# Kernel tuning notes

Hardware: AMD Instinct MI355X
Metric: run time of the kernel (lower is better)

The kernel has to match this reference:

```python
import jax, jax.numpy as jnp
import numpy as np

B = 16384
IN = 1024
H = 1024
LN_EPS = 1e-5


def setup_inputs() -> dict:
    key = jax.random.key(0)
    ks = jax.random.split(key, 8)
    # Five gate Linears fused into one weight [IN+H, 5H] (order: f, i, o, c, m)
    scale = 1.0 / np.sqrt(IN + H)
    W = jax.random.uniform(ks[0], (IN + H, 5 * H), jnp.float32, -scale, scale)
    b = jax.random.uniform(ks[1], (5 * H,), jnp.float32, -scale, scale)
    return {
        "x": jax.random.normal(ks[2], (B, IN), jnp.float32),
        "h_prev": jax.random.normal(ks[3], (B, H), jnp.float32),
        "c_prev": jax.random.normal(ks[4], (B, H), jnp.float32),
        "W": W,
        "b": b,
        "ln_gamma": jnp.ones((H,), jnp.float32),
        "ln_beta": jnp.zeros((H,), jnp.float32),
        "retention": jnp.full((H,), 0.9, jnp.float32),
    }


def _layernorm(z, gamma, beta):
    mu = jnp.mean(z, axis=-1, keepdims=True)
    var = jnp.var(z, axis=-1, keepdims=True)
    return (z - mu) * jax.lax.rsqrt(var + LN_EPS) * gamma + beta


def reference(x, h_prev, c_prev, W, b, ln_gamma, ln_beta, retention):
    combined = jnp.concatenate([x, h_prev], axis=-1)        # [B, IN+H]
    gates = combined @ W + b                                # [B, 5H] fused GEMM
    f_pre, i_pre, o_pre, c_pre_act, m_pre = jnp.split(gates, 5, axis=-1)
    f_gate = jax.nn.sigmoid(f_pre)
    i_gate = jax.nn.sigmoid(i_pre)
    o_gate = jax.nn.sigmoid(o_pre)
    c_cand = jnp.tanh(c_pre_act)
    m_gate = jax.nn.sigmoid(m_pre)
    c_new = f_gate * c_prev + i_gate * c_cand
    c_new = c_new * retention + (1.0 - retention) * c_prev
    c_new = m_gate * c_new + (1.0 - m_gate) * c_prev
    # exp(ln)/(1+exp(ln)) == sigmoid(layernorm(o_gate))
    o_exp = jax.nn.sigmoid(_layernorm(o_gate, ln_gamma, ln_beta))
    h_new = o_exp * jnp.tanh(c_new)
    return h_new, c_new
```

## Files before the change

kernel.cpp:

```cpp
#include <hip/hip_runtime.h>
#include <math.h>


typedef unsigned short u16;
typedef unsigned int   u32;
typedef short  short8 __attribute__((ext_vector_type(8)));
typedef float  f32x4  __attribute__((ext_vector_type(4)));
typedef u16    u16x4  __attribute__((ext_vector_type(4)));
typedef u32    u32x4  __attribute__((ext_vector_type(4)));

#define B_ROWS 16384
#define K_DIM  2048
#define N_DIM  5120
#define H_DIM  1024

__device__ __forceinline__ float b2f(u16 u) {
    u32 v = ((u32)u) << 16;
    return __uint_as_float(v);
}
__device__ __forceinline__ u16 f2b(float f) {
    u32 x = __float_as_uint(f);
    u32 r = (x + 0x7fffu + ((x >> 16) & 1u)) >> 16;
    return (u16)r;
}
__device__ __forceinline__ float sigm(float v) {
    return 1.f / (1.f + __expf(-v));
}
__device__ __forceinline__ float tanh_fast(float v) {
    v = fminf(fmaxf(v, -15.f), 15.f);
    float e = __expf(-2.f * v);
    return (1.f - e) / (1.f + e);
}

__global__ __launch_bounds__(256) void convert_A(const float* __restrict__ x,
                                                 const float* __restrict__ h,
                                                 u16* __restrict__ A) {
    size_t idx = ((size_t)blockIdx.x * 256 + threadIdx.x) * 8;
    int row = (int)(idx >> 11);
    int col = (int)(idx & 2047);
    int srcCol = (col & ~63) | (((((col >> 3) & 7) ^ (row & 7))) << 3);
    const float* src = (srcCol < 1024) ? (x + (size_t)row * 1024 + srcCol)
                                       : (h + (size_t)row * 1024 + (srcCol - 1024));
    f32x4 v0 = *(const f32x4*)src;
    f32x4 v1 = *(const f32x4*)(src + 4);
    u32x4 w;
    w.x = (u32)f2b(v0.x) | ((u32)f2b(v0.y) << 16);
    w.y = (u32)f2b(v0.z) | ((u32)f2b(v0.w) << 16);
    w.z = (u32)f2b(v1.x) | ((u32)f2b(v1.y) << 16);
    w.w = (u32)f2b(v1.z) | ((u32)f2b(v1.w) << 16);
    *(u32x4*)(A + idx) = w;
}

__global__ __launch_bounds__(256) void convert_W(const float* __restrict__ W,
                                                 u16* __restrict__ Wt) {
    __shared__ float tile[64][33];
    const int t  = threadIdx.x;
    const int tx = t & 31;
    const int ty = t >> 5;
    const int n0 = blockIdx.x * 32;
    const int k0 = blockIdx.y * 64;
#pragma unroll
    for (int i = 0; i < 8; ++i)
        tile[ty + 8 * i][tx] = W[(size_t)(k0 + ty + 8 * i) * N_DIM + n0 + tx];
    __syncthreads();
    const int n = t >> 3;
    const int s = t & 7;
    const int g = s ^ (n & 7);
    u32x4 w;
    w.x = (u32)f2b(tile[g * 8 + 0][n]) | ((u32)f2b(tile[g * 8 + 1][n]) << 16);
    w.y = (u32)f2b(tile[g * 8 + 2][n]) | ((u32)f2b(tile[g * 8 + 3][n]) << 16);
    w.z = (u32)f2b(tile[g * 8 + 4][n]) | ((u32)f2b(tile[g * 8 + 5][n]) << 16);
    w.w = (u32)f2b(tile[g * 8 + 6][n]) | ((u32)f2b(tile[g * 8 + 7][n]) << 16);
    *(u32x4*)(Wt + (size_t)(n0 + n) * K_DIM + k0 + s * 8) = w;
}

#define BK 64

__device__ __forceinline__ void gld_lds16(const void* g, void* l) {
    __builtin_amdgcn_global_load_lds(
        (const __attribute__((address_space(1))) void*)g,
        (__attribute__((address_space(3))) void*)l, 16, 0, 0);
}

__global__ __launch_bounds__(512, 2) void gemm_gates(const u16* __restrict__ A,
                                                     const u16* __restrict__ Bt,
                                                     const float* __restrict__ bias,
                                                     u16* __restrict__ gates) {
    __shared__ u16 lds[2][2][256 * BK];

    const int t = threadIdx.x;
    const int bid = blockIdx.x;
    const int swz = (bid & 7) * 160 + (bid >> 3);
    const int m0 = (swz & 63) << 8;
    const int n0 = (swz >> 6) << 8;

    const int l   = t & 63;
    const int wid = t >> 6;
    const int wr  = wid >> 2;
    const int wc  = wid & 3;
    const int lr  = l & 15;
    const int lh  = l >> 4;
    const int z   = lr & 7;
    const int sA0 = (lh ^ z) * 8;

    const int sRow = t >> 3;
    const int sOff = (t & 7) * 8;
    const u16* aBase = A  + (size_t)(m0 + sRow) * K_DIM + sOff;
    const u16* bBase = Bt + (size_t)(n0 + sRow) * K_DIM + sOff;
    const int dOff = t * 8;

    f32x4 acc[8][4] = {};

#define STAGE(kt, buf) do {                                                   \
    _Pragma("unroll") for (int i = 0; i < 4; ++i) {                           \
        gld_lds16(aBase + (size_t)(i * 64) * K_DIM + (kt) * BK,               \
                  &lds[buf][0][dOff + i * 4096]);                             \
        gld_lds16(bBase + (size_t)(i * 64) * K_DIM + (kt) * BK,               \
                  &lds[buf][1][dOff + i * 4096]);                             \
    }                                                                         \
} while (0)

    STAGE(0, 0);

#pragma unroll 1
    for (int kt = 0; kt < 32; ++kt) {
        const int cur = kt & 1;
        if (kt < 31) {
            STAGE(kt + 1, cur ^ 1);
            __builtin_amdgcn_sched_barrier(0);
            asm volatile("s_waitcnt vmcnt(8)" ::: "memory");
        } else {
            __builtin_amdgcn_sched_barrier(0);
            asm volatile("s_waitcnt vmcnt(0)" ::: "memory");
        }
        asm volatile("s_barrier" ::: "memory");
        __builtin_amdgcn_sched_barrier(0);

        const u16* As = lds[cur][0];
        const u16* Bs = lds[cur][1];
        short8 bf[4][2], af[4][2];
#pragma unroll
        for (int ni = 0; ni < 4; ++ni) {
            const int u = (wc * 64 + ni * 16 + lr) * BK;
            bf[ni][0] = *(const short8*)&Bs[u + sA0];
            bf[ni][1] = *(const short8*)&Bs[u + (sA0 ^ 32)];
        }
#pragma unroll
        for (int q = 0; q < 2; ++q) {
#pragma unroll
            for (int m = 0; m < 4; ++m) {
                const int u = (wr * 128 + q * 64 + m * 16 + lr) * BK;
                af[m][0] = *(const short8*)&As[u + sA0];
                af[m][1] = *(const short8*)&As[u + (sA0 ^ 32)];
            }
            __builtin_amdgcn_s_setprio(1);
#pragma unroll
            for (int sk = 0; sk < 2; ++sk)
#pragma unroll
                for (int m = 0; m < 4; ++m)
#pragma unroll
                    for (int ni = 0; ni < 4; ++ni)
                        acc[q * 4 + m][ni] = __builtin_amdgcn_mfma_f32_16x16x32_bf16(
                            af[m][sk], bf[ni][sk], acc[q * 4 + m][ni], 0, 0, 0);
            __builtin_amdgcn_s_setprio(0);
        }

        __builtin_amdgcn_sched_barrier(0);
        asm volatile("s_barrier" ::: "memory");
        __builtin_amdgcn_sched_barrier(0);
    }
#undef STAGE

    const int grp = n0 >> 10;
#pragma unroll
    for (int ni = 0; ni < 4; ++ni) {
        int col = n0 + wc * 64 + ni * 16 + lr;
        float bv = bias[col];
#pragma unroll
        for (int q = 0; q < 2; ++q) {
#pragma unroll
            for (int m = 0; m < 4; ++m) {
#pragma unroll
                for (int j = 0; j < 4; ++j) {
                    int row = m0 + wr * 128 + q * 64 + m * 16 + lh * 4 + j;
                    float v = acc[q * 4 + m][ni][j] + bv;
                    float g = (grp == 3) ? tanh_fast(v) : sigm(v);
                    gates[(size_t)row * N_DIM + col] = f2b(g);
                }
            }
        }
    }
}

__global__ __launch_bounds__(256) void fuse_out(const u16* __restrict__ gates,
                                                const float* __restrict__ c_prev,
                                                const float* __restrict__ ret,
                                                const float* __restrict__ gamma,
                                                const float* __restrict__ beta,
                                                float* __restrict__ out) {
    const int r = blockIdx.x;
    const int t = threadIdx.x;
    const u16* g = gates + (size_t)r * N_DIM;
    const int j0 = t * 4;

    u16x4 ov = *(const u16x4*)(g + 2048 + j0);
    float o0 = b2f(ov.x), o1 = b2f(ov.y), o2 = b2f(ov.z), o3 = b2f(ov.w);
    float s1 = o0 + o1 + o2 + o3;
    float s2 = o0 * o0 + o1 * o1 + o2 * o2 + o3 * o3;
#pragma unroll
    for (int off = 32; off; off >>= 1) {
        s1 += __shfl_xor(s1, off, 64);
        s2 += __shfl_xor(s2, off, 64);
    }
    __shared__ float red[8];
    if ((t & 63) == 0) { red[t >> 6] = s1; red[4 + (t >> 6)] = s2; }
    __syncthreads();
    float S1 = red[0] + red[1] + red[2] + red[3];
    float S2 = red[4] + red[5] + red[6] + red[7];
    float mu   = S1 * (1.f / 1024.f);
    float var  = S2 * (1.f / 1024.f) - mu * mu;
    float rstd = rsqrtf(var + 1e-5f);

    u16x4 fv = *(const u16x4*)(g + j0);
    u16x4 iv = *(const u16x4*)(g + 1024 + j0);
    u16x4 cv = *(const u16x4*)(g + 3072 + j0);
    u16x4 mv = *(const u16x4*)(g + 4096 + j0);
    f32x4 cp = *(const f32x4*)(c_prev + (size_t)r * H_DIM + j0);
    f32x4 rt = *(const f32x4*)(ret + j0);
    f32x4 gm = *(const f32x4*)(gamma + j0);
    f32x4 bt = *(const f32x4*)(beta + j0);

    float of[4] = {o0, o1, o2, o3};
    u16 fa[4] = {fv.x, fv.y, fv.z, fv.w};
    u16 ia[4] = {iv.x, iv.y, iv.z, iv.w};
    u16 ca[4] = {cv.x, cv.y, cv.z, cv.w};
    u16 ma[4] = {mv.x, mv.y, mv.z, mv.w};

    f32x4 hout, cout;
#pragma unroll
    for (int i = 0; i < 4; ++i) {
        float f = b2f(fa[i]), ig = b2f(ia[i]), cc = b2f(ca[i]), m = b2f(ma[i]);
        float cpv = cp[i], rv = rt[i];
        float c1 = f * cpv + ig * cc;
        float c2 = c1 * rv + (1.f - rv) * cpv;
        float cn = m * c2 + (1.f - m) * cpv;
        float ln = (of[i] - mu) * rstd * gm[i] + bt[i];
        float oe = sigm(ln);
        float hn = oe * tanh_fast(cn);
        hout[i] = hn;
        cout[i] = cn;
    }
    *(f32x4*)(out + (size_t)r * H_DIM + j0) = hout;
    *(f32x4*)(out + (size_t)B_ROWS * H_DIM + (size_t)r * H_DIM + j0) = cout;
}

extern "C" void kernel_launch(void* const* d_in, const int* in_sizes, int n_in,
                              void* d_out, int out_size, void* d_ws, size_t ws_size,
                              hipStream_t stream) {
    const float* x      = (const float*)d_in[0];
    const float* h_prev = (const float*)d_in[1];
    const float* c_prev = (const float*)d_in[2];
    const float* W      = (const float*)d_in[3];
    const float* bias   = (const float*)d_in[4];
    const float* gamma  = (const float*)d_in[5];
    const float* beta   = (const float*)d_in[6];
    const float* ret    = (const float*)d_in[7];
    float* out = (float*)d_out;

    u16* Abuf  = (u16*)d_ws;
    u16* Wt    = Abuf + (size_t)B_ROWS * K_DIM;
    u16* gates = Wt + (size_t)N_DIM * K_DIM;

    convert_A<<<(B_ROWS * K_DIM / 8) / 256, 256, 0, stream>>>(x, h_prev, Abuf);
    convert_W<<<dim3(N_DIM / 32, K_DIM / 64), 256, 0, stream>>>(W, Wt);
    gemm_gates<<<(B_ROWS / 256) * (N_DIM / 256), 512, 0, stream>>>(Abuf, Wt, bias, gates);
    fuse_out<<<B_ROWS, 256, 0, stream>>>(gates, c_prev, ret, gamma, beta, out);
}
```

Before: 499.8 us.

## Split GEMM main loop into four half-tile phases interleaving loads and MFMA

Restructures the bf16 gates GEMM main loop from whole-tile double buffering into four phases per k-step. Each phase works on one A half and one B half of the tile and issues the next stage's global-to-LDS load for a matching quarter alongside that phase's MFMA block, with finer barriers and vmcnt/lgkmcnt waits. The goal is to overlap memory traffic with tensor-core work more evenly and to cut register pressure from fragment loads. The trade-off is more barriers per iteration. The final iteration also issues a prefetch past the K extent that is never used.

New measurement: 486.7 us. -2.6%, faster.

```diff
diff --git a/kernel.cpp b/kernel.cpp
--- a/kernel.cpp
+++ b/kernel.cpp
@@ -82,11 +82,19 @@
         (__attribute__((address_space(3))) void*)l, 16, 0, 0);
 }
 
+#define AU(s, h) ((s) * 16384 + (h) * 8192)
+#define BU(s, h) (32768 + (s) * 16384 + (h) * 8192)
+
+#define SBAR()  __builtin_amdgcn_sched_barrier(0)
+#define BAR()   do { SBAR(); asm volatile("s_barrier" ::: "memory"); SBAR(); } while (0)
+#define LGKM0() do { asm volatile("s_waitcnt lgkmcnt(0)" ::: "memory"); SBAR(); } while (0)
+#define VM4()   asm volatile("s_waitcnt vmcnt(4)" ::: "memory")
+
 __global__ __launch_bounds__(512, 2) void gemm_gates(const u16* __restrict__ A,
                                                      const u16* __restrict__ Bt,
                                                      const float* __restrict__ bias,
                                                      u16* __restrict__ gates) {
-    __shared__ u16 lds[2][2][256 * BK];
+    __shared__ u16 lds[65536];
 
     const int t = threadIdx.x;
     const int bid = blockIdx.x;
@@ -103,73 +111,83 @@
     const int z   = lr & 7;
     const int sA0 = (lh ^ z) * 8;
 
-    const int sRow = t >> 3;
-    const int sOff = (t & 7) * 8;
-    const u16* aBase = A  + (size_t)(m0 + sRow) * K_DIM + sOff;
-    const u16* bBase = Bt + (size_t)(n0 + sRow) * K_DIM + sOff;
+    const int tb = t >> 3;
+    const u16* aBase = A  + (size_t)(m0 + tb) * K_DIM + (t & 7) * 8;
+    const u16* bBase = Bt + (size_t)(n0 + (tb & 31) + (tb >> 5) * 64) * K_DIM
+                          + (t & 7) * 8;
     const int dOff = t * 8;
 
     f32x4 acc[8][4] = {};
-
-#define STAGE(kt, buf) do {                                                   \
-    _Pragma("unroll") for (int i = 0; i < 4; ++i) {                           \
-        gld_lds16(aBase + (size_t)(i * 64) * K_DIM + (kt) * BK,               \
-                  &lds[buf][0][dOff + i * 4096]);                             \
-        gld_lds16(bBase + (size_t)(i * 64) * K_DIM + (kt) * BK,               \
-                  &lds[buf][1][dOff + i * 4096]);                             \
+    short8 af[4][2], bf0[2][2], bf1[2][2];
+
+#define STAGE_A(s, h, OFF) do {                                               \
+    gld_lds16(aBase + (size_t)((h) * 64) * K_DIM + (OFF),                     \
+              &lds[AU(s, h) + dOff]);                                         \
+    gld_lds16(aBase + (size_t)((h) * 64 + 128) * K_DIM + (OFF),               \
+              &lds[AU(s, h) + 4096 + dOff]);                                  \
+} while (0)
+#define STAGE_B(s, h, OFF) do {                                               \
+    gld_lds16(bBase + (size_t)((h) * 32) * K_DIM + (OFF),                     \
+              &lds[BU(s, h) + dOff]);                                         \
+    gld_lds16(bBase + (size_t)((h) * 32 + 128) * K_DIM + (OFF),               \
+              &lds[BU(s, h) + 4096 + dOff]);                                  \
+} while (0)
+
+#define RD_AF(s, q) do {                                                      \
+    _Pragma("unroll") for (int m = 0; m < 4; ++m) {                           \
+        const int u_ = AU(s, q) + (wr * 64 + m * 16 + lr) * 64;               \
+        af[m][0] = *(const short8*)&lds[u_ + sA0];                            \
+        af[m][1] = *(const short8*)&lds[u_ + (sA0 ^ 32)];                     \
     }                                                                         \
 } while (0)
-
-    STAGE(0, 0);
+#define RD_BF(dst, s, h) do {                                                 \
+    _Pragma("unroll") for (int n = 0; n < 2; ++n) {                           \
+        const int u_ = BU(s, h) + (wc * 32 + n * 16 + lr) * 64;               \
+        dst[n][0] = *(const short8*)&lds[u_ + sA0];                           \
+        dst[n][1] = *(const short8*)&lds[u_ + (sA0 ^ 32)];                    \
+    }                                                                         \
+} while (0)
+
+#define MFMA16(q, nh, BF) do {                                                \
+    __builtin_amdgcn_s_setprio(1);                                            \
+    _Pragma("unroll") for (int sk = 0; sk < 2; ++sk)                          \
+    _Pragma("unroll") for (int m = 0; m < 4; ++m)                             \
+    _Pragma("unroll") for (int n = 0; n < 2; ++n)                             \
+        acc[(q) * 4 + m][(nh) * 2 + n] =                                      \
+            __builtin_amdgcn_mfma_f32_16x16x32_bf16(                          \
+                af[m][sk], BF[n][sk], acc[(q) * 4 + m][(nh) * 2 + n], 0, 0, 0);\
+    __builtin_amdgcn_s_setprio(0);                                            \
+} while (0)
+
+    STAGE_A(0, 0, 0); STAGE_B(0, 0, 0); STAGE_B(0, 1, 0); STAGE_A(0, 1, 0);
+    SBAR(); VM4(); BAR();
 
 #pragma unroll 1
     for (int kt = 0; kt < 32; ++kt) {
-        const int cur = kt & 1;
-        if (kt < 31) {
-            STAGE(kt + 1, cur ^ 1);
-            __builtin_amdgcn_sched_barrier(0);
-            asm volatile("s_waitcnt vmcnt(8)" ::: "memory");
-        } else {
-            __builtin_amdgcn_sched_barrier(0);
-            asm volatile("s_waitcnt vmcnt(0)" ::: "memory");
-        }
-        asm volatile("s_barrier" ::: "memory");
-        __builtin_amdgcn_sched_barrier(0);
-
-        const u16* As = lds[cur][0];
-        const u16* Bs = lds[cur][1];
-        short8 bf[4][2], af[4][2];
-#pragma unroll
-        for (int ni = 0; ni < 4; ++ni) {
-            const int u = (wc * 64 + ni * 16 + lr) * BK;
-            bf[ni][0] = *(const short8*)&Bs[u + sA0];
-            bf[ni][1] = *(const short8*)&Bs[u + (sA0 ^ 32)];
-        }
-#pragma unroll
-        for (int q = 0; q < 2; ++q) {
-#pragma unroll
-            for (int m = 0; m < 4; ++m) {
-                const int u = (wr * 128 + q * 64 + m * 16 + lr) * BK;
-                af[m][0] = *(const short8*)&As[u + sA0];
-                af[m][1] = *(const short8*)&As[u + (sA0 ^ 32)];
-            }
-            __builtin_amdgcn_s_setprio(1);
-#pragma unroll
-            for (int sk = 0; sk < 2; ++sk)
-#pragma unroll
-                for (int m = 0; m < 4; ++m)
-#pragma unroll
-                    for (int ni = 0; ni < 4; ++ni)
-                        acc[q * 4 + m][ni] = __builtin_amdgcn_mfma_f32_16x16x32_bf16(
-                            af[m][sk], bf[ni][sk], acc[q * 4 + m][ni], 0, 0, 0);
-            __builtin_amdgcn_s_setprio(0);
-        }
-
-        __builtin_amdgcn_sched_barrier(0);
-        asm volatile("s_barrier" ::: "memory");
-        __builtin_amdgcn_sched_barrier(0);
-    }
-#undef STAGE
+        const int s  = kt & 1;
+        const int sp = s ^ 1;
+        const int OFF = (kt + 1) * BK;
+        RD_AF(s, 0); RD_BF(bf0, s, 0); STAGE_A(sp, 0, OFF);
+        BAR(); LGKM0(); MFMA16(0, 0, bf0);
+        VM4();
+        BAR();
+        RD_BF(bf1, s, 1); STAGE_B(sp, 0, OFF);
+        BAR(); LGKM0(); MFMA16(0, 1, bf1);
+        VM4();
+        BAR();
+        RD_AF(s, 1); STAGE_B(sp, 1, OFF);
+        BAR(); LGKM0(); MFMA16(1, 1, bf1);
+        BAR();
+        STAGE_A(sp, 1, OFF);
+        BAR(); MFMA16(1, 0, bf0);
+        VM4();
+        BAR();
+    }
+#undef STAGE_A
+#undef STAGE_B
+#undef RD_AF
+#undef RD_BF
+#undef MFMA16
 
     const int grp = n0 >> 10;
 #pragma unroll
```

## Shrink GEMM tile to 128x256 with BK=32 and triple-buffered LDS pipeline

Applied to the files above, without the earlier changes.

Reworks the gate GEMM to use 128x256 block tiles with a K-step of 32 and a three-stage global->LDS ring buffer, issuing loads two stages ahead with a single barrier per step. The A/W conversion kernels switch to a 4-slot XOR swizzle matching the narrower K tile. The intent is higher occupancy and better latency hiding of global loads; the cost is more barriers per K, smaller per-wave reuse (4x4 MFMA tiles), and tighter register limits from the launch-bounds change.

Result: slower. 510.3 us (+2.1%).

```diff
diff --git a/kernel.cpp b/kernel.cpp
--- a/kernel.cpp
+++ b/kernel.cpp
@@ -38,7 +38,7 @@
     size_t idx = ((size_t)blockIdx.x * 256 + threadIdx.x) * 8;
     int row = (int)(idx >> 11);
     int col = (int)(idx & 2047);
-    int srcCol = (col & ~63) | (((((col >> 3) & 7) ^ (row & 7))) << 3);
+    int srcCol = (col & ~31) | (((((col >> 3) & 3) ^ (row & 3))) << 3);
     const float* src = (srcCol < 1024) ? (x + (size_t)row * 1024 + srcCol)
                                        : (h + (size_t)row * 1024 + (srcCol - 1024));
     f32x4 v0 = *(const f32x4*)src;
@@ -65,16 +65,16 @@
     __syncthreads();
     const int n = t >> 3;
     const int s = t & 7;
-    const int g = s ^ (n & 7);
+    const int g8 = ((s >> 2) << 5) + ((((s & 3) ^ (n & 3))) << 3);
     u32x4 w;
-    w.x = (u32)f2b(tile[g * 8 + 0][n]) | ((u32)f2b(tile[g * 8 + 1][n]) << 16);
-    w.y = (u32)f2b(tile[g * 8 + 2][n]) | ((u32)f2b(tile[g * 8 + 3][n]) << 16);
-    w.z = (u32)f2b(tile[g * 8 + 4][n]) | ((u32)f2b(tile[g * 8 + 5][n]) << 16);
-    w.w = (u32)f2b(tile[g * 8 + 6][n]) | ((u32)f2b(tile[g * 8 + 7][n]) << 16);
+    w.x = (u32)f2b(tile[g8 + 0][n]) | ((u32)f2b(tile[g8 + 1][n]) << 16);
+    w.y = (u32)f2b(tile[g8 + 2][n]) | ((u32)f2b(tile[g8 + 3][n]) << 16);
+    w.z = (u32)f2b(tile[g8 + 4][n]) | ((u32)f2b(tile[g8 + 5][n]) << 16);
+    w.w = (u32)f2b(tile[g8 + 6][n]) | ((u32)f2b(tile[g8 + 7][n]) << 16);
     *(u32x4*)(Wt + (size_t)(n0 + n) * K_DIM + k0 + s * 8) = w;
 }
 
-#define BK 64
+#define BK 32
 
 __device__ __forceinline__ void gld_lds16(const void* g, void* l) {
     __builtin_amdgcn_global_load_lds(
@@ -82,17 +82,21 @@
         (__attribute__((address_space(3))) void*)l, 16, 0, 0);
 }
 
-__global__ __launch_bounds__(512, 2) void gemm_gates(const u16* __restrict__ A,
+#define SB0() __builtin_amdgcn_sched_barrier(0)
+#define BAR() do { SB0(); __builtin_amdgcn_s_barrier(); SB0(); } while (0)
+#define VM3() asm volatile("s_waitcnt vmcnt(3)" ::: "memory")
+
+__global__ __launch_bounds__(512, 4) void gemm_gates(const u16* __restrict__ A,
                                                      const u16* __restrict__ Bt,
                                                      const float* __restrict__ bias,
                                                      u16* __restrict__ gates) {
-    __shared__ u16 lds[2][2][256 * BK];
+    __shared__ u16 lds[3][12288];
 
     const int t = threadIdx.x;
     const int bid = blockIdx.x;
-    const int swz = (bid & 7) * 160 + (bid >> 3);
-    const int m0 = (swz & 63) << 8;
-    const int n0 = (swz >> 6) << 8;
+    const int swz = (bid & 7) * 320 + (bid >> 3);
+    const int m0 = (swz & 127) << 7;
+    const int n0 = (swz >> 7) << 8;
 
     const int l   = t & 63;
     const int wid = t >> 6;
@@ -100,76 +104,53 @@
     const int wc  = wid & 3;
     const int lr  = l & 15;
     const int lh  = l >> 4;
-    const int z   = lr & 7;
-    const int sA0 = (lh ^ z) * 8;
-
-    const int sRow = t >> 3;
-    const int sOff = (t & 7) * 8;
-    const u16* aBase = A  + (size_t)(m0 + sRow) * K_DIM + sOff;
-    const u16* bBase = Bt + (size_t)(n0 + sRow) * K_DIM + sOff;
+    const int slotOff = ((lh ^ (lr & 3)) << 3);
+
+    const u16* aBase = A  + (size_t)(m0 + (t >> 2)) * K_DIM + (t & 3) * 8;
+    const u16* bBase = Bt + (size_t)(n0 + (t >> 2)) * K_DIM + (t & 3) * 8;
     const int dOff = t * 8;
 
-    f32x4 acc[8][4] = {};
-
-#define STAGE(kt, buf) do {                                                   \
-    _Pragma("unroll") for (int i = 0; i < 4; ++i) {                           \
-        gld_lds16(aBase + (size_t)(i * 64) * K_DIM + (kt) * BK,               \
-                  &lds[buf][0][dOff + i * 4096]);                             \
-        gld_lds16(bBase + (size_t)(i * 64) * K_DIM + (kt) * BK,               \
-                  &lds[buf][1][dOff + i * 4096]);                             \
-    }                                                                         \
+    f32x4 acc[4][4] = {};
+    short8 af[4], bf[4];
+
+#define STAGE(Sb, OFF) do {                                                   \
+    gld_lds16(aBase + (OFF),                        &lds[Sb][dOff]);          \
+    gld_lds16(bBase + (OFF),                        &lds[Sb][4096 + dOff]);   \
+    gld_lds16(bBase + (size_t)128 * K_DIM + (OFF),  &lds[Sb][8192 + dOff]);   \
 } while (0)
 
+#define BODY(Rb, Sb, kt) do {                                                 \
+    const int OFF_ = ((kt) + 2) * BK;                                         \
+    STAGE(Sb, OFF_);                                                          \
+    _Pragma("unroll") for (int m = 0; m < 4; ++m)                             \
+        af[m] = *(const short8*)&lds[Rb][(wr * 64 + m * 16 + lr) * 32 + slotOff];\
+    _Pragma("unroll") for (int n = 0; n < 4; ++n)                             \
+        bf[n] = *(const short8*)&lds[Rb][4096 + (wc * 64 + n * 16 + lr) * 32 + slotOff];\
+    _Pragma("unroll") for (int m = 0; m < 4; ++m)                             \
+    _Pragma("unroll") for (int n = 0; n < 4; ++n)                             \
+        acc[m][n] = __builtin_amdgcn_mfma_f32_16x16x32_bf16(                  \
+            af[m], bf[n], acc[m][n], 0, 0, 0);                                \
+    SB0(); VM3();                                                             \
+    __builtin_amdgcn_s_barrier(); SB0();                                      \
+} while (0)
+
     STAGE(0, 0);
+    STAGE(1, BK);
+    SB0(); VM3();
+    __builtin_amdgcn_s_barrier(); SB0();
 
 #pragma unroll 1
-    for (int kt = 0; kt < 32; ++kt) {
-        const int cur = kt & 1;
-        if (kt < 31) {
-            STAGE(kt + 1, cur ^ 1);
-            __builtin_amdgcn_sched_barrier(0);
-            asm volatile("s_waitcnt vmcnt(8)" ::: "memory");
-        } else {
-            __builtin_amdgcn_sched_barrier(0);
-            asm volatile("s_waitcnt vmcnt(0)" ::: "memory");
-        }
-        asm volatile("s_barrier" ::: "memory");
-        __builtin_amdgcn_sched_barrier(0);
-
-        const u16* As = lds[cur][0];
-        const u16* Bs = lds[cur][1];
-        short8 bf[4][2], af[4][2];
-#pragma unroll
-        for (int ni = 0; ni < 4; ++ni) {
-            const int u = (wc * 64 + ni * 16 + lr) * BK;
-            bf[ni][0] = *(const short8*)&Bs[u + sA0];
-            bf[ni][1] = *(const short8*)&Bs[u + (sA0 ^ 32)];
-        }
-#pragma unroll
-        for (int q = 0; q < 2; ++q) {
-#pragma unroll
-            for (int m = 0; m < 4; ++m) {
-                const int u = (wr * 128 + q * 64 + m * 16 + lr) * BK;
-                af[m][0] = *(const short8*)&As[u + sA0];
-                af[m][1] = *(const short8*)&As[u + (sA0 ^ 32)];
-            }
-            __builtin_amdgcn_s_setprio(1);
-#pragma unroll
-            for (int sk = 0; sk < 2; ++sk)
-#pragma unroll
-                for (int m = 0; m < 4; ++m)
-#pragma unroll
-                    for (int ni = 0; ni < 4; ++ni)
-                        acc[q * 4 + m][ni] = __builtin_amdgcn_mfma_f32_16x16x32_bf16(
-                            af[m][sk], bf[ni][sk], acc[q * 4 + m][ni], 0, 0, 0);
-            __builtin_amdgcn_s_setprio(0);
-        }
-
-        __builtin_amdgcn_sched_barrier(0);
-        asm volatile("s_barrier" ::: "memory");
-        __builtin_amdgcn_sched_barrier(0);
-    }
+    for (int it = 0; it < 21; ++it) {
+        const int kt = it * 3;
+        BODY(0, 2, kt);
+        BODY(1, 0, kt + 1);
+        BODY(2, 1, kt + 2);
+    }
+    BODY(0, 2, 63);
 #undef STAGE
+#undef BODY
+
+    asm volatile("s_waitcnt vmcnt(0)" ::: "memory");
 
     const int grp = n0 >> 10;
 #pragma unroll
@@ -177,16 +158,13 @@
         int col = n0 + wc * 64 + ni * 16 + lr;
         float bv = bias[col];
 #pragma unroll
-        for (int q = 0; q < 2; ++q) {
-#pragma unroll
-            for (int m = 0; m < 4; ++m) {
-#pragma unroll
-                for (int j = 0; j < 4; ++j) {
-                    int row = m0 + wr * 128 + q * 64 + m * 16 + lh * 4 + j;
-                    float v = acc[q * 4 + m][ni][j] + bv;
-                    float g = (grp == 3) ? tanh_fast(v) : sigm(v);
-                    gates[(size_t)row * N_DIM + col] = f2b(g);
-                }
+        for (int m = 0; m < 4; ++m) {
+#pragma unroll
+            for (int j = 0; j < 4; ++j) {
+                int row = m0 + wr * 64 + m * 16 + lh * 4 + j;
+                float v = acc[m][ni][j] + bv;
+                float g = (grp == 3) ? tanh_fast(v) : sigm(v);
+                gates[(size_t)row * N_DIM + col] = f2b(g);
             }
         }
     }
@@ -273,6 +251,6 @@
 
     convert_A<<<(B_ROWS * K_DIM / 8) / 256, 256, 0, stream>>>(x, h_prev, Abuf);
     convert_W<<<dim3(N_DIM / 32, K_DIM / 64), 256, 0, stream>>>(W, Wt);
-    gemm_gates<<<(B_ROWS / 256) * (N_DIM / 256), 512, 0, stream>>>(Abuf, Wt, bias, gates);
+    gemm_gates<<<(B_ROWS / 128) * (N_DIM / 256), 512, 0, stream>>>(Abuf, Wt, bias, gates);
     fuse_out<<<B_ROWS, 256, 0, stream>>>(gates, c_prev, ret, gamma, beta, out);
 }
```

## Shrink GEMM tile to 128x128 single-buffered with 4-wave blocks

Applied to the files above, without the earlier changes.

Replaces the 256x256 double-buffered GEMM tile (512 threads, 8 waves, prefetch of the next K-slice with manual waitcnt) with a 128x128 tile, 256 threads, and a single LDS buffer. Each K step loads, syncs, computes and syncs again. The block-to-tile mapping is also rebuilt to group M tiles per XCD. This cuts per-block LDS and registers for higher occupancy, but it drops the load/compute overlap and halves the data reuse per tile, so global and LDS traffic per FLOP rises.

Result: slower. 517.7 us (+3.6%).

```diff
diff --git a/kernel.cpp b/kernel.cpp
--- a/kernel.cpp
+++ b/kernel.cpp
@@ -82,111 +82,84 @@
         (__attribute__((address_space(3))) void*)l, 16, 0, 0);
 }
 
-__global__ __launch_bounds__(512, 2) void gemm_gates(const u16* __restrict__ A,
-                                                     const u16* __restrict__ Bt,
-                                                     const float* __restrict__ bias,
-                                                     u16* __restrict__ gates) {
-    __shared__ u16 lds[2][2][256 * BK];
+__global__ __launch_bounds__(256) void gemm_gates(const u16* __restrict__ A,
+                                                  const u16* __restrict__ Bt,
+                                                  const float* __restrict__ bias,
+                                                  u16* __restrict__ gates) {
+    __shared__ u16 As[128 * BK];
+    __shared__ u16 Bs[128 * BK];
 
     const int t = threadIdx.x;
     const int bid = blockIdx.x;
-    const int swz = (bid & 7) * 160 + (bid >> 3);
-    const int m0 = (swz & 63) << 8;
-    const int n0 = (swz >> 6) << 8;
+    const int xcd = bid & 7;
+    const int c   = bid >> 3;
+    const int m0 = ((xcd << 4) | (c & 15)) << 7;
+    const int n0 = (c >> 4) << 7;
 
     const int l   = t & 63;
     const int wid = t >> 6;
-    const int wr  = wid >> 2;
-    const int wc  = wid & 3;
+    const int wm  = (wid >> 1) << 6;
+    const int wn  = (wid & 1) << 6;
     const int lr  = l & 15;
     const int lh  = l >> 4;
     const int z   = lr & 7;
     const int sA0 = (lh ^ z) * 8;
 
-    const int sRow = t >> 3;
-    const int sOff = (t & 7) * 8;
-    const u16* aBase = A  + (size_t)(m0 + sRow) * K_DIM + sOff;
-    const u16* bBase = Bt + (size_t)(n0 + sRow) * K_DIM + sOff;
+    const int tb = t >> 3;
+    const u16* aPtr = A  + (size_t)(m0 + tb) * K_DIM + (t & 7) * 8;
+    const u16* bPtr = Bt + (size_t)(n0 + tb) * K_DIM + (t & 7) * 8;
     const int dOff = t * 8;
 
-    f32x4 acc[8][4] = {};
-
-#define STAGE(kt, buf) do {                                                   \
-    _Pragma("unroll") for (int i = 0; i < 4; ++i) {                           \
-        gld_lds16(aBase + (size_t)(i * 64) * K_DIM + (kt) * BK,               \
-                  &lds[buf][0][dOff + i * 4096]);                             \
-        gld_lds16(bBase + (size_t)(i * 64) * K_DIM + (kt) * BK,               \
-                  &lds[buf][1][dOff + i * 4096]);                             \
-    }                                                                         \
-} while (0)
-
-    STAGE(0, 0);
+    f32x4 acc[4][4] = {};
 
 #pragma unroll 1
     for (int kt = 0; kt < 32; ++kt) {
-        const int cur = kt & 1;
-        if (kt < 31) {
-            STAGE(kt + 1, cur ^ 1);
-            __builtin_amdgcn_sched_barrier(0);
-            asm volatile("s_waitcnt vmcnt(8)" ::: "memory");
-        } else {
-            __builtin_amdgcn_sched_barrier(0);
-            asm volatile("s_waitcnt vmcnt(0)" ::: "memory");
-        }
-        asm volatile("s_barrier" ::: "memory");
-        __builtin_amdgcn_sched_barrier(0);
-
-        const u16* As = lds[cur][0];
-        const u16* Bs = lds[cur][1];
-        short8 bf[4][2], af[4][2];
-#pragma unroll
-        for (int ni = 0; ni < 4; ++ni) {
-            const int u = (wc * 64 + ni * 16 + lr) * BK;
-            bf[ni][0] = *(const short8*)&Bs[u + sA0];
-            bf[ni][1] = *(const short8*)&Bs[u + (sA0 ^ 32)];
-        }
-#pragma unroll
-        for (int q = 0; q < 2; ++q) {
-#pragma unroll
-            for (int m = 0; m < 4; ++m) {
-                const int u = (wr * 128 + q * 64 + m * 16 + lr) * BK;
-                af[m][0] = *(const short8*)&As[u + sA0];
-                af[m][1] = *(const short8*)&As[u + (sA0 ^ 32)];
-            }
-            __builtin_amdgcn_s_setprio(1);
-#pragma unroll
-            for (int sk = 0; sk < 2; ++sk)
-#pragma unroll
-                for (int m = 0; m < 4; ++m)
-#pragma unroll
-                    for (int ni = 0; ni < 4; ++ni)
-                        acc[q * 4 + m][ni] = __builtin_amdgcn_mfma_f32_16x16x32_bf16(
-                            af[m][sk], bf[ni][sk], acc[q * 4 + m][ni], 0, 0, 0);
-            __builtin_amdgcn_s_setprio(0);
-        }
-
-        __builtin_amdgcn_sched_barrier(0);
-        asm volatile("s_barrier" ::: "memory");
-        __builtin_amdgcn_sched_barrier(0);
-    }
-#undef STAGE
+#pragma unroll
+        for (int i = 0; i < 4; ++i) {
+            gld_lds16(aPtr + (size_t)(i * 32) * K_DIM, &As[i * 2048 + dOff]);
+            gld_lds16(bPtr + (size_t)(i * 32) * K_DIM, &Bs[i * 2048 + dOff]);
+        }
+        __syncthreads();
+
+        short8 af[4][2], bf[4][2];
+#pragma unroll
+        for (int m = 0; m < 4; ++m) {
+            const int u = (wm + m * 16 + lr) * 64;
+            af[m][0] = *(const short8*)&As[u + sA0];
+            af[m][1] = *(const short8*)&As[u + (sA0 ^ 32)];
+        }
+#pragma unroll
+        for (int n = 0; n < 4; ++n) {
+            const int u = (wn + n * 16 + lr) * 64;
+            bf[n][0] = *(const short8*)&Bs[u + sA0];
+            bf[n][1] = *(const short8*)&Bs[u + (sA0 ^ 32)];
+        }
+#pragma unroll
+        for (int sk = 0; sk < 2; ++sk)
+#pragma unroll
+            for (int m = 0; m < 4; ++m)
+#pragma unroll
+                for (int n = 0; n < 4; ++n)
+                    acc[m][n] = __builtin_amdgcn_mfma_f32_16x16x32_bf16(
+                        af[m][sk], bf[n][sk], acc[m][n], 0, 0, 0);
+        __syncthreads();
+        aPtr += BK;
+        bPtr += BK;
+    }
 
     const int grp = n0 >> 10;
 #pragma unroll
     for (int ni = 0; ni < 4; ++ni) {
-        int col = n0 + wc * 64 + ni * 16 + lr;
+        int col = n0 + wn + ni * 16 + lr;
         float bv = bias[col];
 #pragma unroll
-        for (int q = 0; q < 2; ++q) {
-#pragma unroll
-            for (int m = 0; m < 4; ++m) {
-#pragma unroll
-                for (int j = 0; j < 4; ++j) {
-                    int row = m0 + wr * 128 + q * 64 + m * 16 + lh * 4 + j;
-                    float v = acc[q * 4 + m][ni][j] + bv;
-                    float g = (grp == 3) ? tanh_fast(v) : sigm(v);
-                    gates[(size_t)row * N_DIM + col] = f2b(g);
-                }
+        for (int mi = 0; mi < 4; ++mi) {
+#pragma unroll
+            for (int j = 0; j < 4; ++j) {
+                int row = m0 + wm + mi * 16 + lh * 4 + j;
+                float v = acc[mi][ni][j] + bv;
+                float g = (grp == 3) ? tanh_fast(v) : sigm(v);
+                gates[(size_t)row * N_DIM + col] = f2b(g);
             }
         }
     }
@@ -273,6 +246,6 @@
 
     convert_A<<<(B_ROWS * K_DIM / 8) / 256, 256, 0, stream>>>(x, h_prev, Abuf);
     convert_W<<<dim3(N_DIM / 32, K_DIM / 64), 256, 0, stream>>>(W, Wt);
-    gemm_gates<<<(B_ROWS / 256) * (N_DIM / 256), 512, 0, stream>>>(Abuf, Wt, bias, gates);
+    gemm_gates<<<(B_ROWS / 128) * (N_DIM / 128), 256, 0, stream>>>(Abuf, Wt, bias, gates);
     fuse_out<<<B_ROWS, 256, 0, stream>>>(gates, c_prev, ret, gamma, beta, out);
 }
```
